# Optimization experiments

Hardware: AMD Instinct MI355X
Metric: run time of the kernel (lower is better)

The kernel has to match this reference:

```python
import jax, jax.numpy as jnp
import numpy as np

B, S, H, NH, FF = 8, 512, 1024, 16, 4096
DK = H // NH


def _ln(x, g, b):
    m = x.mean(-1, keepdims=True)
    v = ((x - m) ** 2).mean(-1, keepdims=True)
    return (x - m) / jnp.sqrt(v + 1e-5) * g + b


def _fwd(x, predicate_pos, attn_bias, attention_mask, atom_graph, variable_graph,
         ln1_g, ln1_b, wq, bq, wk, bk, wv, bv, wo, bo,
         pq_w, pq_b, pk_w, pk_b, pv_w, pv_b, ln2_g, ln2_b, w1, b1, w2, b2):
    b_, s_, h_ = x.shape
    y = _ln(x, ln1_g, ln1_b)
    # ---- self attention (manual MHA with additive bias + mask) ----
    scale = DK ** -0.5
    q = (y @ wq + bq).reshape(b_, s_, NH, DK) * scale
    k = (y @ wk + bk).reshape(b_, s_, NH, DK)
    v = (y @ wv + bv).reshape(b_, s_, NH, DK)
    scores = jnp.einsum('bihd,bjhd->bhij', q, k)
    scores = scores + attn_bias[:, None, :, :] + attention_mask[:, None, :, :]
    att = jax.nn.softmax(scores, axis=-1)
    y_self = jnp.einsum('bhij,bjhd->bihd', att, v).reshape(b_, s_, h_) @ wo + bo
    # ---- path attention (single-head with graph biases) ----
    pscale = h_ ** -0.5
    pq = (y @ pq_w + pq_b) * pscale
    pk = y @ pk_w + pk_b
    pv = y @ pv_w + pv_b
    patt = jnp.einsum('bid,bjd->bij', pq, pk) + atom_graph + variable_graph
    patt = jax.nn.softmax(patt, axis=-1)
    xp = jnp.einsum('bij,bjd->bid', patt, pv)  # [B,S,H]
    # vectorized gather-mean over predicate positions (replaces per-sample loop)
    prev = jnp.concatenate([xp[:, :1], xp[:, :-1]], axis=1)   # xp[i-1]
    nxt = jnp.concatenate([xp[:, 1:], xp[:, -1:]], axis=1)    # xp[i+1]
    a0 = xp[:, 0:2].mean(axis=1, keepdims=True)               # i == 0
    a1 = xp[:, 0:3].mean(axis=1, keepdims=True)               # i == 1
    a2 = (xp + nxt) / 2.0                                     # pos[i-2] == 1
    a3 = (prev + xp + nxt) / 3.0                              # else
    i_arr = jnp.arange(s_)
    pos = (predicate_pos == 1)
    pos_m2 = jnp.pad(pos[:, :-2], ((0, 0), (2, 0)))           # pos[i-2], False for i<2
    atom = jnp.where(pos_m2[..., None], a2, a3)
    atom = jnp.where((i_arr == 1)[None, :, None], a1, atom)
    atom = jnp.where((i_arr == 0)[None, :, None], a0, atom)
    w = pos.astype(xp.dtype)
    path = (atom * w[..., None]).sum(1) / w.sum(1, keepdims=True)  # [B,H]
    y_path = jnp.broadcast_to(path[:, None, :], (b_, s_, h_))
    # ---- combine + residual + FFN ----
    x = x + (y_self + y_path) / 2.0
    y2 = _ln(x, ln2_g, ln2_b)
    hmid = jax.nn.gelu(y2 @ w1 + b1, approximate=False)
    return x + (hmid @ w2 + b2)


def setup_inputs() -> dict:
    key = jax.random.key(0)
    ks = jax.random.split(key, 16)
    def w(k, shape):
        return 0.02 * jax.random.normal(k, shape, dtype=jnp.float32)
    pp = jax.random.randint(ks[0], (B, S), 0, 2, dtype=jnp.int32)
    pp = pp.at[:, 2].set(1).at[:, -1].set(0)  # >=1 predicate; no predicate at last node
    return {
        'x': jax.random.normal(ks[1], (B, S, H), dtype=jnp.float32),
        'predicate_pos': pp,
        'variable_tags': jnp.zeros((B, S), dtype=jnp.int32),
        'attn_bias': 0.1 * jax.random.normal(ks[2], (B, S, S), dtype=jnp.float32),
        'attention_mask': jnp.zeros((B, S, S), dtype=jnp.float32),
        'atom_graph': 0.1 * jax.random.normal(ks[3], (B, S, S), dtype=jnp.float32),
        'variable_graph': 0.1 * jax.random.normal(ks[4], (B, S, S), dtype=jnp.float32),
        'ln1_g': jnp.ones((H,), jnp.float32), 'ln1_b': jnp.zeros((H,), jnp.float32),
        'wq': w(ks[5], (H, H)), 'bq': jnp.zeros((H,), jnp.float32),
        'wk': w(ks[6], (H, H)), 'bk': jnp.zeros((H,), jnp.float32),
        'wv': w(ks[7], (H, H)), 'bv': jnp.zeros((H,), jnp.float32),
        'wo': w(ks[8], (H, H)), 'bo': jnp.zeros((H,), jnp.float32),
        'pq_w': w(ks[9], (H, H)), 'pq_b': jnp.zeros((H,), jnp.float32),
        'pk_w': w(ks[10], (H, H)), 'pk_b': jnp.zeros((H,), jnp.float32),
        'pv_w': w(ks[11], (H, H)), 'pv_b': jnp.zeros((H,), jnp.float32),
        'ln2_g': jnp.ones((H,), jnp.float32), 'ln2_b': jnp.zeros((H,), jnp.float32),
        'w1': w(ks[12], (H, FF)), 'b1': jnp.zeros((FF,), jnp.float32),
        'w2': w(ks[13], (FF, H)), 'b2': jnp.zeros((H,), jnp.float32),
    }


def reference(x, predicate_pos, variable_tags, attn_bias, attention_mask, atom_graph, variable_graph,
              ln1_g, ln1_b, wq, bq, wk, bk, wv, bv, wo, bo,
              pq_w, pq_b, pk_w, pk_b, pv_w, pv_b, ln2_g, ln2_b, w1, b1, w2, b2):
    # variable_tags is unused in the original forward as well
    return _fwd(x, predicate_pos, attn_bias, attention_mask, atom_graph, variable_graph,
                ln1_g, ln1_b, wq, bq, wk, bk, wv, bv, wo, bo,
                pq_w, pq_b, pk_w, pk_b, pv_w, pv_b, ln2_g, ln2_b, w1, b1, w2, b2)
```

## Files before the change

### kernel.cpp

```cpp
#include <hip/hip_runtime.h>
#include <hip/hip_bf16.h>
#include <math.h>


typedef __bf16 bf16x8 __attribute__((ext_vector_type(8)));
typedef float f32x4 __attribute__((ext_vector_type(4)));

__device__ __forceinline__ void async_copy16(void* lds, const void* g) {
  __builtin_amdgcn_global_load_lds(
      (__attribute__((address_space(1))) void*)(void*)g,
      (__attribute__((address_space(3))) void*)lds, 16, 0, 0);
}

#define SB0 __builtin_amdgcn_sched_barrier(0)
#define BARRIER __builtin_amdgcn_s_barrier()

__global__ __launch_bounds__(256) void ln_rows_bf16(
    const float* __restrict__ X, const float* __restrict__ G,
    const float* __restrict__ Bt, __hip_bfloat16* __restrict__ O) {
  long row = blockIdx.x;
  int t = threadIdx.x;
  const float4 xv = ((const float4*)(X + row * 1024))[t];
  float s = xv.x + xv.y + xv.z + xv.w;
  float q = xv.x * xv.x + xv.y * xv.y + xv.z * xv.z + xv.w * xv.w;
#pragma unroll
  for (int o = 32; o; o >>= 1) {
    s += __shfl_xor(s, o);
    q += __shfl_xor(q, o);
  }
  __shared__ float rs[4], rq[4];
  int wid = t >> 6;
  if ((t & 63) == 0) { rs[wid] = s; rq[wid] = q; }
  __syncthreads();
  s = rs[0] + rs[1] + rs[2] + rs[3];
  q = rq[0] + rq[1] + rq[2] + rq[3];
  float mean = s * (1.f / 1024.f);
  float var = q * (1.f / 1024.f) - mean * mean;
  float rstd = rsqrtf(var + 1e-5f);
  const float4 gv = ((const float4*)G)[t];
  const float4 bv = ((const float4*)Bt)[t];
  __hip_bfloat16* o = O + row * 1024 + t * 4;
  o[0] = __float2bfloat16((xv.x - mean) * rstd * gv.x + bv.x);
  o[1] = __float2bfloat16((xv.y - mean) * rstd * gv.y + bv.y);
  o[2] = __float2bfloat16((xv.z - mean) * rstd * gv.z + bv.z);
  o[3] = __float2bfloat16((xv.w - mean) * rstd * gv.w + bv.w);
}

struct TC7 {
  const float* in[7];
  __hip_bfloat16* out[7];
  float scale[7];
};
__global__ __launch_bounds__(256) void tconv7(TC7 p) {
  __shared__ float t[32][33];
  int j = blockIdx.z;
  const float* in = p.in[j];
  __hip_bfloat16* out = p.out[j];
  float sc = p.scale[j];
  int c0 = blockIdx.x * 32, r0 = blockIdx.y * 32;
  int tid = threadIdx.x;
  int lr = tid >> 3, lc = (tid & 7) * 4;
  const float4 v = *(const float4*)&in[(long)(r0 + lr) * 1024 + c0 + lc];
  t[lr][lc] = v.x; t[lr][lc + 1] = v.y; t[lr][lc + 2] = v.z; t[lr][lc + 3] = v.w;
  __syncthreads();
  int oc = tid >> 3, orr = (tid & 7) * 4;
  __hip_bfloat16* o = &out[(long)(c0 + oc) * 1024 + r0 + orr];
  o[0] = __float2bfloat16(t[orr][oc] * sc);
  o[1] = __float2bfloat16(t[orr + 1][oc] * sc);
  o[2] = __float2bfloat16(t[orr + 2][oc] * sc);
  o[3] = __float2bfloat16(t[orr + 3][oc] * sc);
}

__global__ __launch_bounds__(256) void tconv_f32_bf16(
    const float* __restrict__ in, __hip_bfloat16* __restrict__ out, int R,
    int C) {
  __shared__ float t[32][33];
  int c0 = blockIdx.x * 32, r0 = blockIdx.y * 32;
  int tid = threadIdx.x;
  int lr = tid >> 3, lc = (tid & 7) * 4;
  const float4 v = *(const float4*)&in[(long)(r0 + lr) * C + c0 + lc];
  t[lr][lc] = v.x; t[lr][lc + 1] = v.y; t[lr][lc + 2] = v.z; t[lr][lc + 3] = v.w;
  __syncthreads();
  int oc = tid >> 3, orr = (tid & 7) * 4;
  __hip_bfloat16* o = &out[(long)(c0 + oc) * R + r0 + orr];
  o[0] = __float2bfloat16(t[orr][oc]);
  o[1] = __float2bfloat16(t[orr + 1][oc]);
  o[2] = __float2bfloat16(t[orr + 2][oc]);
  o[3] = __float2bfloat16(t[orr + 3][oc]);
}

__global__ __launch_bounds__(256) void tconv_bf16(
    const __hip_bfloat16* __restrict__ in, __hip_bfloat16* __restrict__ out,
    int R, int C, int ldin, long sIn) {
  __shared__ __hip_bfloat16 t[32][34];
  int bz = blockIdx.z;
  long ibase = (long)bz * sIn;
  long obase = (long)bz * R * C;
  int c0 = blockIdx.x * 32, r0 = blockIdx.y * 32;
  int tid = threadIdx.x;
  int lr = tid >> 3, lc = (tid & 7) * 4;
  const __hip_bfloat16* ip = &in[ibase + (long)(r0 + lr) * ldin + c0 + lc];
  t[lr][lc] = ip[0]; t[lr][lc + 1] = ip[1]; t[lr][lc + 2] = ip[2]; t[lr][lc + 3] = ip[3];
  __syncthreads();
  int oc = tid >> 3, orr = (tid & 7) * 4;
  __hip_bfloat16* o = &out[obase + (long)(c0 + oc) * R + r0 + orr];
  o[0] = t[orr][oc];
  o[1] = t[orr + 1][oc];
  o[2] = t[orr + 2][oc];
  o[3] = t[orr + 3][oc];
}

struct BC6 {
  const float* b[6];
  float scale[6];
};
__global__ __launch_bounds__(256) void bias_concat(BC6 p, float* __restrict__ o) {
  int idx = blockIdx.x * 256 + threadIdx.x;
  int j = idx >> 10, e = idx & 1023;
  o[idx] = p.b[j][e] * p.scale[j];
}

template <int BN>
__global__ __launch_bounds__(512, 2) void gemm256(
    const __hip_bfloat16* __restrict__ A, const __hip_bfloat16* __restrict__ Bt,
    const float* __restrict__ bias, void* __restrict__ C, int K, int lda,
    int ldb, int ldc, int act, int obf, long sC) {
  constexpr int NR = BN / 64;
  constexpr int ABYTES = 256 * 128;
  constexpr int BBYTES = BN * 128;
  constexpr int BUF = ABYTES + BBYTES;
  __shared__ char lds[2 * BUF];

  int bx, by;
  {
    int wg = blockIdx.y * gridDim.x + blockIdx.x;
    int gx = gridDim.x, gy = gridDim.y;
    if ((gx & 3) == 0 && (gy & 1) == 0) {
      int cw = gx >> 2, ch = gy >> 1;
      int xcd = wg & 7, idx = wg >> 3;
      bx = (xcd & 3) * cw + idx % cw;
      by = (xcd >> 2) * ch + idx / cw;
    } else {
      bx = blockIdx.x;
      by = blockIdx.y;
    }
  }
  const int m0 = by * 256, n0 = bx * BN;
  const int z = blockIdx.z;
  const long kbase = (long)z * K * 2;

  const int tid = threadIdx.x;
  const int lane = tid & 63, wid = tid >> 6;
  const int wm = wid >> 2, wn = wid & 3;
  const int ll = lane & 15, lh = lane >> 4;

  const char* Ag = (const char*)A;
  const char* Bg = (const char*)Bt;
  const int srow = tid >> 3;
  const int scb = (((tid & 7) ^ (srow & 7)) << 4);
  const int sld = (tid & 7) << 4;

  auto stageA = [&](char* base, long kb) {
#pragma unroll
    for (int l = 0; l < 4; ++l) {
      int row = l * 64 + srow;
      async_copy16(base + row * 128 + sld,
                   Ag + ((long)(m0 + row) * lda) * 2 + kb + scb);
    }
  };
  auto stageB = [&](char* base, long kb) {
#pragma unroll
    for (int l = 0; l < BN / 64; ++l) {
      int row = l * 64 + srow;
      async_copy16(base + ABYTES + row * 128 + sld,
                   Bg + ((long)(n0 + row) * ldb) * 2 + kb + scb);
    }
  };

  const int rx = ll & 7;
  const int ck[2] = {((0 + lh) ^ rx) << 4, ((4 + lh) ^ rx) << 4};

  f32x4 acc[8][NR];
#pragma unroll
  for (int m = 0; m < 8; ++m)
#pragma unroll
    for (int n = 0; n < NR; ++n) acc[m][n] = (f32x4){0.f, 0.f, 0.f, 0.f};

  const int nt = K >> 6;
  stageA(lds, kbase);
  stageB(lds, kbase);

  for (int t = 0; t < nt; ++t) {
    const int bt = t & 1;
    const char* Ab = lds + bt * BUF;
    const char* Bb = Ab + ABYTES;
    char* nb = lds + (bt ^ 1) * BUF;
    const bool pre = (t + 1 < nt);

    SB0; BARRIER; SB0;
    if (pre) {
      const long kb = kbase + (long)(t + 1) * 128;
      stageA(nb, kb);
      stageB(nb, kb);
      if constexpr (BN == 256)
        asm volatile("s_waitcnt vmcnt(8)" ::: "memory");
      else if constexpr (BN == 192)
        asm volatile("s_waitcnt vmcnt(7)" ::: "memory");
      else
        asm volatile("s_waitcnt vmcnt(6)" ::: "memory");
    } else {
      asm volatile("s_waitcnt vmcnt(0)" ::: "memory");
    }
    SB0; BARRIER; SB0;

#pragma unroll
    for (int ks = 0; ks < 2; ++ks) {
      bf16x8 bf[NR];
#pragma unroll
      for (int n = 0; n < NR; ++n)
        bf[n] = *(const bf16x8*)(Bb + (wn * (BN / 4) + n * 16 + ll) * 128 +
                                 ck[ks]);
      bf16x8 af[4];
#pragma unroll
      for (int m = 0; m < 4; ++m)
        af[m] = *(const bf16x8*)(Ab + (wm * 128 + m * 16 + ll) * 128 + ck[ks]);
      __builtin_amdgcn_s_setprio(1);
#pragma unroll
      for (int m = 0; m < 4; ++m)
#pragma unroll
        for (int n = 0; n < NR; ++n)
          acc[m][n] = __builtin_amdgcn_mfma_f32_16x16x32_bf16(af[m], bf[n],
                                                              acc[m][n], 0, 0, 0);
      __builtin_amdgcn_s_setprio(0);
#pragma unroll
      for (int m = 0; m < 4; ++m)
        af[m] = *(const bf16x8*)(Ab + (wm * 128 + (m + 4) * 16 + ll) * 128 +
                                 ck[ks]);
      __builtin_amdgcn_s_setprio(1);
#pragma unroll
      for (int m = 0; m < 4; ++m)
#pragma unroll
        for (int n = 0; n < NR; ++n)
          acc[m + 4][n] = __builtin_amdgcn_mfma_f32_16x16x32_bf16(
              af[m], bf[n], acc[m + 4][n], 0, 0, 0);
      __builtin_amdgcn_s_setprio(0);
    }
  }

#pragma unroll
  for (int m = 0; m < 8; ++m) {
    int row = m0 + wm * 128 + m * 16 + lh * 4;
#pragma unroll
    for (int n = 0; n < NR; ++n) {
      int col = n0 + wn * (BN / 4) + n * 16 + ll;
      float bs = bias ? bias[col] : 0.f;
#pragma unroll
      for (int r = 0; r < 4; ++r) {
        float v = acc[m][n][r] + bs;
        if (act) v = v * 0.5f * (1.f + erff(v * 0.70710678118f));
        long cidx = (long)z * sC + (long)(row + r) * ldc + col;
        if (obf)
          ((__hip_bfloat16*)C)[cidx] = __float2bfloat16(v);
        else
          ((float*)C)[cidx] = v;
      }
    }
  }
}

__global__ __launch_bounds__(256) void ffn2_reduce(
    const float* __restrict__ P, const float* __restrict__ X2,
    const float* __restrict__ b2, float* __restrict__ OUT) {
  int i = blockIdx.x * 256 + threadIdx.x;
  const long SP = 4194304;
  float4 a = ((const float4*)P)[i];
  float4 b = ((const float4*)(P + SP))[i];
  float4 c = ((const float4*)(P + 2 * SP))[i];
  float4 d = ((const float4*)(P + 3 * SP))[i];
  float4 xr = ((const float4*)X2)[i];
  const float4 bb = *(const float4*)(b2 + ((i & 255) * 4));
  float4 o;
  o.x = a.x + b.x + c.x + d.x + xr.x + bb.x;
  o.y = a.y + b.y + c.y + d.y + xr.y + bb.y;
  o.z = a.z + b.z + c.z + d.z + xr.z + bb.z;
  o.w = a.w + b.w + c.w + d.w + xr.w + bb.w;
  ((float4*)OUT)[i] = o;
}

__global__ __launch_bounds__(256) void gemm_bf16_nt(
    const __hip_bfloat16* __restrict__ A, const __hip_bfloat16* __restrict__ Bt,
    const float* __restrict__ bias, const float* __restrict__ E1,
    const float* __restrict__ E2, void* __restrict__ C, int K, int lda,
    int ldb, int ldc, long sA, long sB, long sC, long sE, float alpha, int act,
    int obf, int pbc, int ksplit, long sSplit) {
  __shared__ unsigned short AsU[2][128 * 32];
  __shared__ unsigned short BsU[2][128 * 32];
  const int tid = threadIdx.x;
  const int lane = tid & 63, wave = tid >> 6;
  const int wr = wave >> 1, wc = wave & 1;

  int nwg = gridDim.x * gridDim.y;
  int wg = blockIdx.y * gridDim.x + blockIdx.x;
  int bx = blockIdx.x, by = blockIdx.y;
  if ((nwg & 7) == 0) {
    int cpx = nwg >> 3;
    int sw = (wg & 7) * cpx + (wg >> 3);
    bx = sw % gridDim.x;
    by = sw / gridDim.x;
  }
  const int m0 = by * 128, n0 = bx * 128;
  const int bz = blockIdx.z / ksplit;
  const int sk = blockIdx.z % ksplit;
  if (sk != 0) { bias = nullptr; E1 = nullptr; E2 = nullptr; }
  const int kcol0 = sk * K;
  const char* Ab = (const char*)(A + (long)bz * sA);
  const char* Bb = (const char*)(Bt + (long)bz * sB);

  f32x4 acc[4][4];
#pragma unroll
  for (int m = 0; m < 4; ++m)
#pragma unroll
    for (int n = 0; n < 4; ++n) acc[m][n] = (f32x4){0.f, 0.f, 0.f, 0.f};

  const int srow = tid >> 2;
  const int scol = (tid & 3) * 16;
  const int wbase = (tid >> 6) * 1024;

  auto stage = [&](int buf, int k0) {
    int kk = kcol0 + k0;
#pragma unroll
    for (int i = 0; i < 2; ++i) {
      async_copy16((char*)AsU[buf] + i * 4096 + wbase,
                   Ab + ((long)(m0 + i * 64 + srow) * lda + kk) * 2 + scol);
      async_copy16((char*)BsU[buf] + i * 4096 + wbase,
                   Bb + ((long)(n0 + i * 64 + srow) * ldb + kk) * 2 + scol);
    }
  };

  const int ntk = K >> 5;
  stage(0, 0);

  for (int t = 0; t < ntk; ++t) {
    const int bt = t & 1;
    SB0; BARRIER; SB0;
    if (t + 1 < ntk) {
      stage(bt ^ 1, (t + 1) * 32);
      asm volatile("s_waitcnt vmcnt(4)" ::: "memory");
    } else {
      asm volatile("s_waitcnt vmcnt(0)" ::: "memory");
    }
    SB0; BARRIER; SB0;

    const int koff = (lane >> 4) * 8;
    bf16x8 a[4], b[4];
#pragma unroll
    for (int m = 0; m < 4; ++m)
      a[m] = *(const bf16x8*)&AsU[bt][(wr * 64 + m * 16 + (lane & 15)) * 32 +
                                      koff];
#pragma unroll
    for (int n = 0; n < 4; ++n)
      b[n] = *(const bf16x8*)&BsU[bt][(wc * 64 + n * 16 + (lane & 15)) * 32 +
                                      koff];
    __builtin_amdgcn_s_setprio(1);
#pragma unroll
    for (int m = 0; m < 4; ++m)
#pragma unroll
      for (int n = 0; n < 4; ++n)
        acc[m][n] = __builtin_amdgcn_mfma_f32_16x16x32_bf16(a[m], b[n],
                                                            acc[m][n], 0, 0, 0);
    __builtin_amdgcn_s_setprio(0);
  }

#pragma unroll
  for (int m = 0; m < 4; ++m) {
    int row = m0 + wr * 64 + m * 16 + (lane >> 4) * 4;
#pragma unroll
    for (int n = 0; n < 4; ++n) {
      int col = n0 + wc * 64 + n * 16 + (lane & 15);
      float bs = bias ? bias[col] : 0.f;
#pragma unroll
      for (int r = 0; r < 4; ++r) {
        float v = (acc[m][n][r] + bs) * alpha;
        if (pbc) {
          v = E1[(long)(row + r) * ldc + col] +
              0.5f * (v + E2[(long)((row + r) >> 9) * 1024 + col]);
        } else {
          long eidx = (long)bz * sE + (long)(row + r) * ldc + col;
          if (E1) v += E1[eidx];
          if (E2) v += E2[eidx];
        }
        if (act) v = v * 0.5f * (1.f + erff(v * 0.70710678118f));
        long cidx = (long)bz * sC + (long)sk * sSplit +
                    (long)(row + r) * ldc + col;
        if (obf)
          ((__hip_bfloat16*)C)[cidx] = __float2bfloat16(v);
        else
          ((float*)C)[cidx] = v;
      }
    }
  }
}

__global__ __launch_bounds__(256) void attn_mfma(
    const __hip_bfloat16* __restrict__ Q, const __hip_bfloat16* __restrict__ K,
    const __hip_bfloat16* __restrict__ VT, const float* __restrict__ BiasP,
    const float* __restrict__ MaskP, __hip_bfloat16* __restrict__ O,
    int ldqk) {
  __shared__ __hip_bfloat16 P[32][520];
  __shared__ float red[2][32][4];
  const int it = blockIdx.x, h = blockIdx.y, b = blockIdx.z;
  const int i0 = it * 32;
  const int tid = threadIdx.x;
  const int lane = tid & 63, w = tid >> 6;
  const int lh = lane >> 4, ll = lane & 15;

  const long qkb = (long)b * 512 * ldqk + h * 64;

  bf16x8 a[2][2];
#pragma unroll
  for (int m = 0; m < 2; ++m)
#pragma unroll
    for (int ks = 0; ks < 2; ++ks)
      a[m][ks] = *(const bf16x8*)&Q[qkb + (long)(i0 + m * 16 + ll) * ldqk +
                                    ks * 32 + lh * 8];

  f32x4 acc[2][8];
#pragma unroll
  for (int m = 0; m < 2; ++m)
#pragma unroll
    for (int n = 0; n < 8; ++n) acc[m][n] = (f32x4){0.f, 0.f, 0.f, 0.f};

#pragma unroll
  for (int n = 0; n < 8; ++n) {
    const __hip_bfloat16* kp =
        &K[qkb + (long)(w * 128 + n * 16 + ll) * ldqk + lh * 8];
    bf16x8 b0 = *(const bf16x8*)&kp[0];
    bf16x8 b1 = *(const bf16x8*)&kp[32];
#pragma unroll
    for (int m = 0; m < 2; ++m) {
      acc[m][n] =
          __builtin_amdgcn_mfma_f32_16x16x32_bf16(a[m][0], b0, acc[m][n], 0, 0, 0);
      acc[m][n] =
          __builtin_amdgcn_mfma_f32_16x16x32_bf16(a[m][1], b1, acc[m][n], 0, 0, 0);
    }
  }

  const long bmo = ((long)b * 512 + i0) * 512 + w * 128;
#pragma unroll
  for (int m = 0; m < 2; ++m)
#pragma unroll
    for (int r = 0; r < 4; ++r) {
      int row = m * 16 + lh * 4 + r;
#pragma unroll
      for (int n = 0; n < 8; ++n) {
        long gi = bmo + (long)row * 512 + n * 16 + ll;
        acc[m][n][r] += BiasP[gi] + MaskP[gi];
      }
    }

  float rmax[2][4];
#pragma unroll
  for (int m = 0; m < 2; ++m)
#pragma unroll
    for (int r = 0; r < 4; ++r) {
      float v = acc[m][0][r];
#pragma unroll
      for (int n = 1; n < 8; ++n) v = fmaxf(v, acc[m][n][r]);
#pragma unroll
      for (int o = 1; o < 16; o <<= 1) v = fmaxf(v, __shfl_xor(v, o));
      rmax[m][r] = v;
    }
  if (ll == 0) {
#pragma unroll
    for (int m = 0; m < 2; ++m)
#pragma unroll
      for (int r = 0; r < 4; ++r) red[0][m * 16 + lh * 4 + r][w] = rmax[m][r];
  }
  __syncthreads();
#pragma unroll
  for (int m = 0; m < 2; ++m)
#pragma unroll
    for (int r = 0; r < 4; ++r) {
      const float* p = red[0][m * 16 + lh * 4 + r];
      rmax[m][r] = fmaxf(fmaxf(p[0], p[1]), fmaxf(p[2], p[3]));
    }
  float rsum[2][4];
#pragma unroll
  for (int m = 0; m < 2; ++m)
#pragma unroll
    for (int r = 0; r < 4; ++r) {
      float s = 0.f;
#pragma unroll
      for (int n = 0; n < 8; ++n) {
        float e = __expf(acc[m][n][r] - rmax[m][r]);
        acc[m][n][r] = e;
        s += e;
      }
#pragma unroll
      for (int o = 1; o < 16; o <<= 1) s += __shfl_xor(s, o);
      rsum[m][r] = s;
    }
  if (ll == 0) {
#pragma unroll
    for (int m = 0; m < 2; ++m)
#pragma unroll
      for (int r = 0; r < 4; ++r) red[1][m * 16 + lh * 4 + r][w] = rsum[m][r];
  }
  __syncthreads();
#pragma unroll
  for (int m = 0; m < 2; ++m)
#pragma unroll
    for (int r = 0; r < 4; ++r) {
      const float* p = red[1][m * 16 + lh * 4 + r];
      float inv = 1.f / (p[0] + p[1] + p[2] + p[3]);
      int row = m * 16 + lh * 4 + r;
#pragma unroll
      for (int n = 0; n < 8; ++n)
        P[row][w * 128 + n * 16 + ll] = __float2bfloat16(acc[m][n][r] * inv);
    }
  __syncthreads();

  const long vtb = ((long)b * 1024 + h * 64) * 512;
  const long ob = (long)b * 512 * 1024 + h * 64;
  const int mw = (w >> 1) * 16, nw = (w & 1) * 32;
  f32x4 oacc[2];
  oacc[0] = (f32x4){0.f, 0.f, 0.f, 0.f};
  oacc[1] = (f32x4){0.f, 0.f, 0.f, 0.f};
#pragma unroll
  for (int ks = 0; ks < 16; ++ks) {
    int k0 = ks * 32;
    bf16x8 pa = *(const bf16x8*)&P[mw + ll][k0 + lh * 8];
#pragma unroll
    for (int nf = 0; nf < 2; ++nf) {
      bf16x8 vb = *(const bf16x8*)&VT[vtb + (long)(nw + nf * 16 + ll) * 512 +
                                      k0 + lh * 8];
      oacc[nf] =
          __builtin_amdgcn_mfma_f32_16x16x32_bf16(pa, vb, oacc[nf], 0, 0, 0);
    }
  }
#pragma unroll
  for (int nf = 0; nf < 2; ++nf)
#pragma unroll
    for (int r = 0; r < 4; ++r)
      O[ob + (long)(i0 + mw + lh * 4 + r) * 1024 + nw + nf * 16 + ll] =
          __float2bfloat16(oacc[nf][r]);
}

__global__ __launch_bounds__(256) void softmax_rows2(
    const float* __restrict__ P0, const float* __restrict__ P1,
    __hip_bfloat16* __restrict__ Ob) {
  const float* r0 = P0 + (long)blockIdx.x * 512;
  const float* r1 = P1 + (long)blockIdx.x * 512;
  __hip_bfloat16* orow = Ob + (long)blockIdx.x * 512;
  int t = threadIdx.x;
  float v0 = r0[t] + r1[t], v1 = r0[t + 256] + r1[t + 256];
  float m = fmaxf(v0, v1);
#pragma unroll
  for (int o = 32; o; o >>= 1) m = fmaxf(m, __shfl_xor(m, o));
  __shared__ float red[8];
  int wid = t >> 6, lane = t & 63;
  if (!lane) red[wid] = m;
  __syncthreads();
  m = fmaxf(fmaxf(red[0], red[1]), fmaxf(red[2], red[3]));
  float e0 = __expf(v0 - m), e1 = __expf(v1 - m);
  float s = e0 + e1;
#pragma unroll
  for (int o = 32; o; o >>= 1) s += __shfl_xor(s, o);
  if (!lane) red[4 + wid] = s;
  __syncthreads();
  s = red[4] + red[5] + red[6] + red[7];
  float inv = 1.f / s;
  orow[t] = __float2bfloat16(e0 * inv);
  orow[t + 256] = __float2bfloat16(e1 * inv);
}

__global__ __launch_bounds__(256) void path_partial(
    const float* __restrict__ xp, const int* __restrict__ pp,
    float* __restrict__ PP, float* __restrict__ WS) {
  int b = blockIdx.x, hc = blockIdx.y, ic = blockIdx.z;
  int h = hc * 256 + threadIdx.x;
  const int* ppb = pp + b * 512;
  const float* xb = xp + (long)b * 512 * 1024;
  int iA = ic * 64, iB = iA + 64;
  float acc = 0.f;
  for (int i = iA; i < iB; ++i) {
    if (ppb[i] != 1) continue;
    float cur = xb[(long)i * 1024 + h];
    float a;
    if (i == 0) {
      a = 0.5f * (cur + xb[1024 + h]);
    } else if (i == 1) {
      a = (xb[h] + cur + xb[2 * 1024 + h]) * (1.f / 3.f);
    } else {
      int inx = (i + 1 < 512) ? i + 1 : 511;
      float nx = xb[(long)inx * 1024 + h];
      if (ppb[i - 2] == 1) {
        a = 0.5f * (cur + nx);
      } else {
        a = (xb[(long)(i - 1) * 1024 + h] + cur + nx) * (1.f / 3.f);
      }
    }
    acc += a;
  }
  PP[((long)b * 8 + ic) * 1024 + h] = acc;
  if (hc == 0 && threadIdx.x == 0) {
    float c = 0.f;
    for (int i = iA; i < iB; ++i) c += (ppb[i] == 1) ? 1.f : 0.f;
    WS[b * 8 + ic] = c;
  }
}

__global__ __launch_bounds__(256) void path_finalize(
    const float* __restrict__ PP, const float* __restrict__ WS,
    float* __restrict__ PATH) {
  int b = blockIdx.x;
  int h = blockIdx.y * 256 + threadIdx.x;
  float s = 0.f, w = 0.f;
#pragma unroll
  for (int ic = 0; ic < 8; ++ic) {
    s += PP[((long)b * 8 + ic) * 1024 + h];
    w += WS[b * 8 + ic];
  }
  PATH[b * 1024 + h] = s / w;
}

extern "C" void kernel_launch(void* const* d_in, const int* in_sizes, int n_in,
                              void* d_out, int out_size, void* d_ws,
                              size_t ws_size, hipStream_t stream) {
  const float* x = (const float*)d_in[0];
  const int* pp = (const int*)d_in[1];
  const float* abias = (const float*)d_in[3];
  const float* amask = (const float*)d_in[4];
  const float* agraph = (const float*)d_in[5];
  const float* vgraph = (const float*)d_in[6];
  const float* ln1g = (const float*)d_in[7];
  const float* ln1b = (const float*)d_in[8];
  const float* wq = (const float*)d_in[9];
  const float* bq = (const float*)d_in[10];
  const float* wk = (const float*)d_in[11];
  const float* bk = (const float*)d_in[12];
  const float* wv = (const float*)d_in[13];
  const float* bv = (const float*)d_in[14];
  const float* wo = (const float*)d_in[15];
  const float* bo = (const float*)d_in[16];
  const float* pqw = (const float*)d_in[17];
  const float* pqb = (const float*)d_in[18];
  const float* pkw = (const float*)d_in[19];
  const float* pkb = (const float*)d_in[20];
  const float* pvw = (const float*)d_in[21];
  const float* pvb = (const float*)d_in[22];
  const float* ln2g = (const float*)d_in[23];
  const float* ln2b = (const float*)d_in[24];
  const float* w1 = (const float*)d_in[25];
  const float* b1 = (const float*)d_in[26];
  const float* w2 = (const float*)d_in[27];
  const float* b2 = (const float*)d_in[28];

  char* wsb = (char*)d_ws;
  auto Ybf = (__hip_bfloat16*)(wsb);
  auto QKV = (__hip_bfloat16*)(wsb + (8l << 20));
  auto VTb = (__hip_bfloat16*)(wsb + (56l << 20));
  auto PVT = (__hip_bfloat16*)(wsb + (64l << 20));
  auto ATTb = (__hip_bfloat16*)(wsb + (72l << 20));
  auto PATTb = (__hip_bfloat16*)(wsb + (88l << 20));
  auto PATTf = (float*)(wsb + (92l << 20));
  auto XP = (float*)(wsb + (92l << 20));
  auto WALL = (__hip_bfloat16*)(wsb + (108l << 20));
  auto WOT = (__hip_bfloat16*)(wsb + (120l << 20));
  auto W1T = (__hip_bfloat16*)(wsb + (122l << 20));
  auto bias6 = (float*)(wsb + (130l << 20));
  auto PPart = (float*)(wsb + (131l << 20));
  auto WSp = (float*)(wsb + (132l << 20));
  auto PATH = (float*)(wsb + (133l << 20));
  auto X2 = (float*)(wsb + (24l << 20));
  auto HMID = (__hip_bfloat16*)(wsb + (40l << 20));
  auto W2T = ATTb;
  auto PART = (float*)(wsb + (92l << 20));
  __hip_bfloat16* Y2b = Ybf;
  float* OUT = (float*)d_out;

  const float qscale = 0.125f;
  const float pscale = 0.03125f;
  const long S2 = 512l * 512;
  const long SQ = 512l * 6144;
  const long SPLT = 8l * S2;

  __hip_bfloat16* Qp = QKV;
  __hip_bfloat16* Kp = QKV + 1024;
  __hip_bfloat16* Vp = QKV + 2048;
  __hip_bfloat16* PQp = QKV + 3072;
  __hip_bfloat16* PKp = QKV + 4096;
  __hip_bfloat16* PVp = QKV + 5120;

  TC7 tp;
  tp.in[0] = wq;  tp.out[0] = WALL;                 tp.scale[0] = qscale;
  tp.in[1] = wk;  tp.out[1] = WALL + 1024 * 1024;   tp.scale[1] = 1.f;
  tp.in[2] = wv;  tp.out[2] = WALL + 2048 * 1024;   tp.scale[2] = 1.f;
  tp.in[3] = pqw; tp.out[3] = WALL + 3072 * 1024;   tp.scale[3] = pscale;
  tp.in[4] = pkw; tp.out[4] = WALL + 4096 * 1024;   tp.scale[4] = 1.f;
  tp.in[5] = pvw; tp.out[5] = WALL + 5120 * 1024;   tp.scale[5] = 1.f;
  tp.in[6] = wo;  tp.out[6] = WOT;                  tp.scale[6] = 1.f;
  tconv7<<<dim3(32, 32, 7), 256, 0, stream>>>(tp);
  tconv_f32_bf16<<<dim3(128, 32), 256, 0, stream>>>(w1, W1T, 1024, 4096);

  BC6 bp;
  bp.b[0] = bq;  bp.scale[0] = qscale;
  bp.b[1] = bk;  bp.scale[1] = 1.f;
  bp.b[2] = bv;  bp.scale[2] = 1.f;
  bp.b[3] = pqb; bp.scale[3] = pscale;
  bp.b[4] = pkb; bp.scale[4] = 1.f;
  bp.b[5] = pvb; bp.scale[5] = 1.f;
  bias_concat<<<24, 256, 0, stream>>>(bp, bias6);

  ln_rows_bf16<<<4096, 256, 0, stream>>>(x, ln1g, ln1b, Ybf);

  gemm256<192><<<dim3(32, 16, 1), 512, 0, stream>>>(
      Ybf, WALL, bias6, QKV, 1024, 1024, 1024, 6144, 0, 1, 0);

  tconv_bf16<<<dim3(32, 16, 8), 256, 0, stream>>>(Vp, VTb, 512, 1024, 6144, SQ);
  tconv_bf16<<<dim3(32, 16, 8), 256, 0, stream>>>(PVp, PVT, 512, 1024, 6144, SQ);

  gemm_bf16_nt<<<dim3(4, 4, 16), 256, 0, stream>>>(
      PQp, PKp, nullptr, agraph, vgraph, PATTf, 512, 6144, 6144, 512, SQ, SQ,
      S2, S2, 1.f, 0, 0, 0, 2, SPLT);
  softmax_rows2<<<4096, 256, 0, stream>>>(PATTf, PATTf + SPLT, PATTb);

  attn_mfma<<<dim3(16, 16, 8), 256, 0, stream>>>(Qp, Kp, VTb, abias, amask,
                                                 ATTb, 6144);

  gemm_bf16_nt<<<dim3(8, 4, 8), 256, 0, stream>>>(
      PATTb, PVT, nullptr, nullptr, nullptr, XP, 512, 512, 512, 1024, S2,
      512l * 1024, 512l * 1024, 0, 1.f, 0, 0, 0, 1, 0);

  path_partial<<<dim3(8, 4, 8), 256, 0, stream>>>(XP, pp, PPart, WSp);
  path_finalize<<<dim3(8, 4), 256, 0, stream>>>(PPart, WSp, PATH);

  gemm_bf16_nt<<<dim3(8, 32, 1), 256, 0, stream>>>(
      ATTb, WOT, bo, x, PATH, X2, 1024, 1024, 1024, 1024, 0, 0, 0, 0, 1.f, 0,
      0, 1, 1, 0);

  tconv_f32_bf16<<<dim3(32, 128), 256, 0, stream>>>(w2, W2T, 4096, 1024);

  ln_rows_bf16<<<4096, 256, 0, stream>>>(X2, ln2g, ln2b, Y2b);

  gemm256<256><<<dim3(16, 16, 1), 512, 0, stream>>>(
      Y2b, W1T, b1, HMID, 1024, 1024, 1024, 4096, 1, 1, 0);

  gemm256<256><<<dim3(4, 16, 4), 512, 0, stream>>>(
      HMID, W2T, nullptr, PART, 1024, 4096, 4096, 1024, 0, 0, 4194304);

  ffn2_reduce<<<4096, 256, 0, stream>>>(PART, X2, b2, OUT);
}
```

Before: 452.4 us.

## Halve GEMM K-tile to BK=32 and raise occupancy to four blocks per CU

The templated 256xBN GEMM becomes a fixed 256x256 tile with a K-step of 32 instead of 64. This halves LDS use per block and raises launch bounds from 2 to 4 blocks per CU. The swizzle and staging pattern are reworked for 64-byte rows, and the QKV projection now uses 256-wide N tiles on a 24x16 grid. The aim is more occupancy to hide latency, at the cost of twice as many barrier-synchronised iterations and tighter register limits that may cause spills with the 8x4 accumulator array.

```diff
diff --git a/kernel.cpp b/kernel.cpp
--- a/kernel.cpp
+++ b/kernel.cpp
@@ -120,14 +120,12 @@
   o[idx] = p.b[j][e] * p.scale[j];
 }
 
-template <int BN>
-__global__ __launch_bounds__(512, 2) void gemm256(
+__global__ __launch_bounds__(512, 4) void gemm256(
     const __hip_bfloat16* __restrict__ A, const __hip_bfloat16* __restrict__ Bt,
     const float* __restrict__ bias, void* __restrict__ C, int K, int lda,
     int ldb, int ldc, int act, int obf, long sC) {
-  constexpr int NR = BN / 64;
-  constexpr int ABYTES = 256 * 128;
-  constexpr int BBYTES = BN * 128;
+  constexpr int ABYTES = 256 * 64;
+  constexpr int BBYTES = 256 * 64;
   constexpr int BUF = ABYTES + BBYTES;
   __shared__ char lds[2 * BUF];
 
@@ -145,7 +143,7 @@
       by = blockIdx.y;
     }
   }
-  const int m0 = by * 256, n0 = bx * BN;
+  const int m0 = by * 256, n0 = bx * 256;
   const int z = blockIdx.z;
   const long kbase = (long)z * K * 2;
 
@@ -156,103 +154,86 @@
 
   const char* Ag = (const char*)A;
   const char* Bg = (const char*)Bt;
-  const int srow = tid >> 3;
-  const int scb = (((tid & 7) ^ (srow & 7)) << 4);
-  const int sld = (tid & 7) << 4;
-
-  auto stageA = [&](char* base, long kb) {
-#pragma unroll
-    for (int l = 0; l < 4; ++l) {
-      int row = l * 64 + srow;
-      async_copy16(base + row * 128 + sld,
+  const int srow = tid >> 2;
+  const int scb = (((tid & 3) ^ (srow & 3)) << 4);
+  const int sld = (tid & 3) << 4;
+
+  auto stage = [&](char* base, long kb) {
+#pragma unroll
+    for (int l = 0; l < 2; ++l) {
+      int row = l * 128 + srow;
+      async_copy16(base + row * 64 + sld,
                    Ag + ((long)(m0 + row) * lda) * 2 + kb + scb);
     }
+#pragma unroll
+    for (int l = 0; l < 2; ++l) {
+      int row = l * 128 + srow;
+      async_copy16(base + ABYTES + row * 64 + sld,
+                   Bg + ((long)(n0 + row) * ldb) * 2 + kb + scb);
+    }
   };
-  auto stageB = [&](char* base, long kb) {
-#pragma unroll
-    for (int l = 0; l < BN / 64; ++l) {
-      int row = l * 64 + srow;
-      async_copy16(base + ABYTES + row * 128 + sld,
-                   Bg + ((long)(n0 + row) * ldb) * 2 + kb + scb);
-    }
-  };
-
-  const int rx = ll & 7;
-  const int ck[2] = {((0 + lh) ^ rx) << 4, ((4 + lh) ^ rx) << 4};
-
-  f32x4 acc[8][NR];
+
+  const int ckk = ((lh ^ (ll & 3)) << 4);
+
+  f32x4 acc[8][4];
 #pragma unroll
   for (int m = 0; m < 8; ++m)
 #pragma unroll
-    for (int n = 0; n < NR; ++n) acc[m][n] = (f32x4){0.f, 0.f, 0.f, 0.f};
-
-  const int nt = K >> 6;
-  stageA(lds, kbase);
-  stageB(lds, kbase);
+    for (int n = 0; n < 4; ++n) acc[m][n] = (f32x4){0.f, 0.f, 0.f, 0.f};
+
+  const int nt = K >> 5;
+  stage(lds, kbase);
 
   for (int t = 0; t < nt; ++t) {
     const int bt = t & 1;
     const char* Ab = lds + bt * BUF;
     const char* Bb = Ab + ABYTES;
     char* nb = lds + (bt ^ 1) * BUF;
-    const bool pre = (t + 1 < nt);
 
     SB0; BARRIER; SB0;
-    if (pre) {
-      const long kb = kbase + (long)(t + 1) * 128;
-      stageA(nb, kb);
-      stageB(nb, kb);
-      if constexpr (BN == 256)
-        asm volatile("s_waitcnt vmcnt(8)" ::: "memory");
-      else if constexpr (BN == 192)
-        asm volatile("s_waitcnt vmcnt(7)" ::: "memory");
-      else
-        asm volatile("s_waitcnt vmcnt(6)" ::: "memory");
+    if (t + 1 < nt) {
+      stage(nb, kbase + (long)(t + 1) * 64);
+      asm volatile("s_waitcnt vmcnt(4)" ::: "memory");
     } else {
       asm volatile("s_waitcnt vmcnt(0)" ::: "memory");
     }
     SB0; BARRIER; SB0;
 
-#pragma unroll
-    for (int ks = 0; ks < 2; ++ks) {
-      bf16x8 bf[NR];
-#pragma unroll
-      for (int n = 0; n < NR; ++n)
-        bf[n] = *(const bf16x8*)(Bb + (wn * (BN / 4) + n * 16 + ll) * 128 +
-                                 ck[ks]);
-      bf16x8 af[4];
-#pragma unroll
-      for (int m = 0; m < 4; ++m)
-        af[m] = *(const bf16x8*)(Ab + (wm * 128 + m * 16 + ll) * 128 + ck[ks]);
-      __builtin_amdgcn_s_setprio(1);
-#pragma unroll
-      for (int m = 0; m < 4; ++m)
-#pragma unroll
-        for (int n = 0; n < NR; ++n)
-          acc[m][n] = __builtin_amdgcn_mfma_f32_16x16x32_bf16(af[m], bf[n],
-                                                              acc[m][n], 0, 0, 0);
-      __builtin_amdgcn_s_setprio(0);
-#pragma unroll
-      for (int m = 0; m < 4; ++m)
-        af[m] = *(const bf16x8*)(Ab + (wm * 128 + (m + 4) * 16 + ll) * 128 +
-                                 ck[ks]);
-      __builtin_amdgcn_s_setprio(1);
-#pragma unroll
-      for (int m = 0; m < 4; ++m)
-#pragma unroll
-        for (int n = 0; n < NR; ++n)
-          acc[m + 4][n] = __builtin_amdgcn_mfma_f32_16x16x32_bf16(
-              af[m], bf[n], acc[m + 4][n], 0, 0, 0);
-      __builtin_amdgcn_s_setprio(0);
-    }
+    bf16x8 bf[4];
+#pragma unroll
+    for (int n = 0; n < 4; ++n)
+      bf[n] = *(const bf16x8*)(Bb + (wn * 64 + n * 16 + ll) * 64 + ckk);
+    bf16x8 af[4];
+#pragma unroll
+    for (int m = 0; m < 4; ++m)
+      af[m] = *(const bf16x8*)(Ab + (wm * 128 + m * 16 + ll) * 64 + ckk);
+    __builtin_amdgcn_s_setprio(1);
+#pragma unroll
+    for (int m = 0; m < 4; ++m)
+#pragma unroll
+      for (int n = 0; n < 4; ++n)
+        acc[m][n] = __builtin_amdgcn_mfma_f32_16x16x32_bf16(af[m], bf[n],
+                                                            acc[m][n], 0, 0, 0);
+    __builtin_amdgcn_s_setprio(0);
+#pragma unroll
+    for (int m = 0; m < 4; ++m)
+      af[m] = *(const bf16x8*)(Ab + (wm * 128 + (m + 4) * 16 + ll) * 64 + ckk);
+    __builtin_amdgcn_s_setprio(1);
+#pragma unroll
+    for (int m = 0; m < 4; ++m)
+#pragma unroll
+      for (int n = 0; n < 4; ++n)
+        acc[m + 4][n] = __builtin_amdgcn_mfma_f32_16x16x32_bf16(
+            af[m], bf[n], acc[m + 4][n], 0, 0, 0);
+    __builtin_amdgcn_s_setprio(0);
   }
 
 #pragma unroll
   for (int m = 0; m < 8; ++m) {
     int row = m0 + wm * 128 + m * 16 + lh * 4;
 #pragma unroll
-    for (int n = 0; n < NR; ++n) {
-      int col = n0 + wn * (BN / 4) + n * 16 + ll;
+    for (int n = 0; n < 4; ++n) {
+      int col = n0 + wn * 64 + n * 16 + ll;
       float bs = bias ? bias[col] : 0.f;
 #pragma unroll
       for (int r = 0; r < 4; ++r) {
@@ -714,7 +695,7 @@
 
   ln_rows_bf16<<<4096, 256, 0, stream>>>(x, ln1g, ln1b, Ybf);
 
-  gemm256<192><<<dim3(32, 16, 1), 512, 0, stream>>>(
+  gemm256<<<dim3(24, 16, 1), 512, 0, stream>>>(
       Ybf, WALL, bias6, QKV, 1024, 1024, 1024, 6144, 0, 1, 0);
 
   tconv_bf16<<<dim3(32, 16, 8), 256, 0, stream>>>(Vp, VTb, 512, 1024, 6144, SQ);
@@ -743,10 +724,10 @@
 
   ln_rows_bf16<<<4096, 256, 0, stream>>>(X2, ln2g, ln2b, Y2b);
 
-  gemm256<256><<<dim3(16, 16, 1), 512, 0, stream>>>(
+  gemm256<<<dim3(16, 16, 1), 512, 0, stream>>>(
       Y2b, W1T, b1, HMID, 1024, 1024, 1024, 4096, 1, 1, 0);
 
-  gemm256<256><<<dim3(4, 16, 4), 512, 0, stream>>>(
+  gemm256<<<dim3(4, 16, 4), 512, 0, stream>>>(
       HMID, W2T, nullptr, PART, 1024, 4096, 4096, 1024, 0, 0, 4194304);
 
   ffn2_reduce<<<4096, 256, 0, stream>>>(PART, X2, b2, OUT);
```

Result: slower. 1.562 ms (+245.4%).
